# Performance work log

Hardware: AMD Instinct MI355X
Metric: run time of the kernel (lower is better)

Reference implementation:

```python
import jax, jax.numpy as jnp
import numpy as np
from jax import lax

B, T, D = 1024, 100, 12
NEG_SLOPE = 0.01  # torch.nn.LeakyReLU default


def setup_inputs() -> dict:
    key = jax.random.key(0)
    ks = jax.random.split(key, 6)
    y0 = jax.random.normal(ks[0], (B, T, D), dtype=jnp.float32)
    # shared, increasing time grid per row (forward only uses row 0, made relative)
    t = jnp.broadcast_to(jnp.linspace(0.0, 1.0, T, dtype=jnp.float32), (B, T)) + 0.0
    def lin(k, fan_in, fan_out):
        s = 1.0 / np.sqrt(fan_in)
        return jax.random.normal(k, (fan_in, fan_out), dtype=jnp.float32) * s
    W1 = lin(ks[1], D, 300); b1 = jnp.zeros((300,), jnp.float32)
    W2 = lin(ks[2], 300, 100); b2 = jnp.zeros((100,), jnp.float32)
    W3 = lin(ks[3], 100, 50); b3 = jnp.zeros((50,), jnp.float32)
    W4 = lin(ks[4], 50, D); b4 = jnp.zeros((D,), jnp.float32)
    return {"y0": y0, "t": t, "W1": W1, "b1": b1, "W2": W2, "b2": b2,
            "W3": W3, "b3": b3, "W4": W4, "b4": b4}


def _mlp(x, W1, b1, W2, b2, W3, b3, W4, b4):
    h = jax.nn.leaky_relu(x @ W1 + b1, NEG_SLOPE)
    h = jax.nn.leaky_relu(h @ W2 + b2, NEG_SLOPE)
    h = jax.nn.leaky_relu(h @ W3 + b3, NEG_SLOPE)
    return h @ W4 + b4


def reference(y0, t, W1, b1, W2, b2, W3, b3, W4, b4):
    # t_span: relative times of batch row 0 (as in the torch forward)
    t_rel = t[0] - t[0, 0]                       # [T]
    x0 = y0[:, 0, :]                             # [B, D] initial state
    f = lambda x: _mlp(x, W1, b1, W2, b2, W3, b3, W4, b4)

    def rk4_step(x, dt):
        k1 = f(x)
        k2 = f(x + 0.5 * dt * k1)
        k3 = f(x + 0.5 * dt * k2)
        k4 = f(x + dt * k3)
        x_new = x + (dt / 6.0) * (k1 + 2.0 * k2 + 2.0 * k3 + k4)
        return x_new, x_new

    dts = t_rel[1:] - t_rel[:-1]                 # [T-1]
    _, traj = lax.scan(rk4_step, x0, dts)        # [T-1, B, D]
    traj = jnp.concatenate([x0[None], traj], axis=0)  # [T, B, D]
    return jnp.swapaxes(traj, 0, 1)              # [B, T, D]
```

## Files before the change

kernel.cpp:

```cpp
#include <hip/hip_runtime.h>


typedef float v2f __attribute__((ext_vector_type(2)));
typedef float v4f __attribute__((ext_vector_type(4)));

constexpr int TT = 100;
constexpr int D  = 12;
constexpr int H1 = 300;
constexpr int H2 = 100;
constexpr int H3 = 50;
constexpr float NEG = 0.01f;

__device__ __forceinline__ float lrelu(float x) { return fmaxf(x, NEG * x); }
__device__ __forceinline__ v2f lo2(v4f v) { return __builtin_shufflevector(v, v, 0, 1); }
__device__ __forceinline__ v2f hi2(v4f v) { return __builtin_shufflevector(v, v, 2, 3); }
__device__ __forceinline__ v2f pkfma(v2f a, v2f b, v2f c) {
#if __has_builtin(__builtin_elementwise_fma)
    return __builtin_elementwise_fma(a, b, c);
#else
    return a * b + c;
#endif
}

__global__ __launch_bounds__(512)
void node_rk4_kernel(const float* __restrict__ y0, const float* __restrict__ t,
                     const float* __restrict__ W1, const float* __restrict__ b1,
                     const float* __restrict__ W2, const float* __restrict__ b2,
                     const float* __restrict__ W3, const float* __restrict__ b3,
                     const float* __restrict__ W4, const float* __restrict__ b4,
                     float* __restrict__ out)
{
    __shared__ __align__(16) float sW3c[25 * 200];
    __shared__ __align__(16) float sW4 [52 * 12];
    __shared__ __align__(16) float h1T [304 * 4];
    __shared__ __align__(16) float pL2 [32 * 104];
    __shared__ __align__(16) float h2e [4 * 104];
    __shared__ __align__(16) float h3e [4 * 52];
    __shared__ __align__(16) float sx  [48];
    __shared__ __align__(16) float sxe [48];
    __shared__ __align__(16) float sks [48];
    __shared__ float sb2[100];
    __shared__ float st [100];

    const int tid = threadIdx.x;
    const int l   = tid & 63;
    const int w   = tid >> 6;
    const bool l2act = (l < 50);

    const bool l1act = (tid < H1);
    float w1v[12];
    float rb1 = 0.0f;
#pragma unroll
    for (int k = 0; k < 12; ++k) w1v[k] = 0.0f;
    if (l1act) {
        rb1 = b1[tid];
#pragma unroll
        for (int k = 0; k < 12; ++k) w1v[k] = W1[k * H1 + tid];
    }

    float w2a[38], w2b[38];
#pragma unroll
    for (int i = 0; i < 38; ++i) {
        const int k = w * 38 + i;
        float va = 0.0f, vb = 0.0f;
        if (l2act && k < H1) { va = W2[k * H2 + l]; vb = W2[k * H2 + l + 50]; }
        w2a[i] = va; w2b[i] = vb;
    }

    const float rb3 = (w < 4 && l < 50) ? b3[l] : 0.0f;

    const int u4 = tid - 256;
    const bool l4act = (u4 >= 0 && u4 < 192);
    int e4 = 0, j4 = 0, kq4 = 0;
    float b4v = 0.0f;
    if (l4act) {
        e4 = u4 / 48; const int r = u4 - e4 * 48; j4 = r >> 2; kq4 = r & 3;
        b4v = b4[j4];
    }

    for (int i = tid; i < H2 * H3; i += 512) {
        const int k = i / H3, j = i - k * H3;
        sW3c[(k >> 2) * 200 + j * 4 + (k & 3)] = W3[i];
    }
    for (int i = tid; i < 52 * 12; i += 512) sW4[i] = (i < H3 * D) ? W4[i] : 0.0f;
    if (tid < H2) sb2[tid] = b2[tid];
    if (tid < TT) st[tid] = t[tid];
    if (tid >= 104 && tid < 120) h1T[300 * 4 + (tid - 104)] = 0.0f;
    if (tid >= 120 && tid < 128) {
        const int u = tid - 120;
        h3e[(u >> 1) * 52 + 50 + (u & 1)] = 0.0f;
    }
    if (tid < 48) {
        const int e = tid / 12, j = tid - e * 12;
        const int g = (blockIdx.x * 4 + e) * (TT * D) + j;
        const float v = y0[g];
        sx[tid] = v;
        out[g]  = v;
    }
    __syncthreads();

    for (int s = 0; s < TT - 1; ++s) {
#pragma unroll 1
        for (int ev = 0; ev < 4; ++ev) {
            const float* xin = ev ? sxe : sx;

            if (l1act) {
                v4f r;
#pragma unroll
                for (int e = 0; e < 4; ++e) {
                    const v4f x0 = *(const v4f*)(xin + e * 12);
                    const v4f x1 = *(const v4f*)(xin + e * 12 + 4);
                    const v4f x2 = *(const v4f*)(xin + e * 12 + 8);
                    float a = rb1;
                    a = fmaf(x0.x, w1v[0], a);  a = fmaf(x0.y, w1v[1], a);
                    a = fmaf(x0.z, w1v[2], a);  a = fmaf(x0.w, w1v[3], a);
                    a = fmaf(x1.x, w1v[4], a);  a = fmaf(x1.y, w1v[5], a);
                    a = fmaf(x1.z, w1v[6], a);  a = fmaf(x1.w, w1v[7], a);
                    a = fmaf(x2.x, w1v[8], a);  a = fmaf(x2.y, w1v[9], a);
                    a = fmaf(x2.z, w1v[10], a); a = fmaf(x2.w, w1v[11], a);
                    r[e] = lrelu(a);
                }
                *(v4f*)(h1T + tid * 4) = r;
            }
            __syncthreads();

            {
                v2f a01A = {0,0}, a23A = {0,0}, a01B = {0,0}, a23B = {0,0};
                const float* hb = h1T + w * (38 * 4);
#pragma unroll
                for (int i = 0; i < 38; ++i) {
                    const v4f hv = *(const v4f*)(hb + i * 4);
                    const v2f wA = {w2a[i], w2a[i]};
                    const v2f wB = {w2b[i], w2b[i]};
                    a01A = pkfma(lo2(hv), wA, a01A);
                    a23A = pkfma(hi2(hv), wA, a23A);
                    a01B = pkfma(lo2(hv), wB, a01B);
                    a23B = pkfma(hi2(hv), wB, a23B);
                }
                if (l2act) {
                    pL2[(w * 4 + 0) * 104 + l]      = a01A.x;
                    pL2[(w * 4 + 1) * 104 + l]      = a01A.y;
                    pL2[(w * 4 + 2) * 104 + l]      = a23A.x;
                    pL2[(w * 4 + 3) * 104 + l]      = a23A.y;
                    pL2[(w * 4 + 0) * 104 + l + 50] = a01B.x;
                    pL2[(w * 4 + 1) * 104 + l + 50] = a01B.y;
                    pL2[(w * 4 + 2) * 104 + l + 50] = a23B.x;
                    pL2[(w * 4 + 3) * 104 + l + 50] = a23B.y;
                }
            }
            __syncthreads();

            if (tid < 400) {
                const int e = tid / 100, j = tid - e * 100;
                float v = sb2[j];
#pragma unroll
                for (int q = 0; q < 8; ++q) v += pL2[(q * 4 + e) * 104 + j];
                h2e[e * 104 + j] = lrelu(v);
            }
            __syncthreads();

            if (w < 4 && l2act) {
                v2f acc = {0, 0};
                const float* hb2 = h2e + w * 104;
                const float* wb  = sW3c + l * 4;
#pragma unroll
                for (int c = 0; c < 25; ++c) {
                    const v4f wv = *(const v4f*)(wb + c * 200);
                    const v4f hv = *(const v4f*)(hb2 + c * 4);
                    acc = pkfma(lo2(hv), lo2(wv), acc);
                    acc = pkfma(hi2(hv), hi2(wv), acc);
                }
                h3e[w * 52 + l] = lrelu(acc.x + acc.y + rb3);
            }
            __syncthreads();

            if (l4act) {
                const int kb = kq4 * 13;
                float a = 0.0f;
                const float* hb3 = h3e + e4 * 52 + kb;
#pragma unroll
                for (int i = 0; i < 13; ++i)
                    a = fmaf(hb3[i], sW4[(kb + i) * 12 + j4], a);
                a += __shfl_xor(a, 1);
                a += __shfl_xor(a, 2);
                if (kq4 == 0) {
                    a += b4v;
                    const float dt = st[s + 1] - st[s];
                    const int bi = e4 * 12 + j4;
                    const float xc = sx[bi];
                    if (ev == 0)      { sks[bi] = a;        sxe[bi] = xc + 0.5f * dt * a; }
                    else if (ev == 1) { sks[bi] += 2.f * a; sxe[bi] = xc + 0.5f * dt * a; }
                    else if (ev == 2) { sks[bi] += 2.f * a; sxe[bi] = xc + dt * a; }
                    else {
                        const float xn = xc + dt * (1.0f / 6.0f) * (sks[bi] + a);
                        sx[bi] = xn;
                        out[(blockIdx.x * 4 + e4) * (TT * D) + (s + 1) * D + j4] = xn;
                    }
                }
            }
            __syncthreads();
        }
    }
}

extern "C" void kernel_launch(void* const* d_in, const int* in_sizes, int n_in,
                              void* d_out, int out_size, void* d_ws, size_t ws_size,
                              hipStream_t stream) {
    const float* y0 = (const float*)d_in[0];
    const float* t  = (const float*)d_in[1];
    const float* W1 = (const float*)d_in[2];
    const float* b1 = (const float*)d_in[3];
    const float* W2 = (const float*)d_in[4];
    const float* b2 = (const float*)d_in[5];
    const float* W3 = (const float*)d_in[6];
    const float* b3 = (const float*)d_in[7];
    const float* W4 = (const float*)d_in[8];
    const float* b4 = (const float*)d_in[9];
    float* out = (float*)d_out;

    node_rk4_kernel<<<256, 512, 0, stream>>>(y0, t, W1, b1, W2, b2, W3, b3, W4, b4, out);
}
```

Before: 1.308 ms.

## Double block size, split layer-2 reduction wider, fuse tail layers per wave

The block grows to 1024 threads, so each wave handles 19 rows of the layer-2 K dimension instead of 38. Partial sums are stored in an element-major layout that can be reduced with vector loads. The layer-2 reduction, layer 3, layer 4 and the RK4 update are merged into one stage run by four waves, one per batch element. This removes two block-wide barriers per function evaluation. The RK accumulator and state now live in registers instead of shared memory. The trade-off is heavier register pressure from the 1024-thread launch bound, and the tail stage relies on lockstep execution within a wave for its shared-memory handoffs.

```diff
diff --git a/kernel.cpp b/kernel.cpp
--- a/kernel.cpp
+++ b/kernel.cpp
@@ -22,7 +22,7 @@
 #endif
 }
 
-__global__ __launch_bounds__(512)
+__global__ __launch_bounds__(1024)
 void node_rk4_kernel(const float* __restrict__ y0, const float* __restrict__ t,
                      const float* __restrict__ W1, const float* __restrict__ b1,
                      const float* __restrict__ W2, const float* __restrict__ b2,
@@ -33,13 +33,11 @@
     __shared__ __align__(16) float sW3c[25 * 200];
     __shared__ __align__(16) float sW4 [52 * 12];
     __shared__ __align__(16) float h1T [304 * 4];
-    __shared__ __align__(16) float pL2 [32 * 104];
+    __shared__ __align__(16) float pL2v[4 * 100 * 20];
     __shared__ __align__(16) float h2e [4 * 104];
     __shared__ __align__(16) float h3e [4 * 52];
     __shared__ __align__(16) float sx  [48];
     __shared__ __align__(16) float sxe [48];
-    __shared__ __align__(16) float sks [48];
-    __shared__ float sb2[100];
     __shared__ float st [100];
 
     const int tid = threadIdx.x;
@@ -47,6 +45,15 @@
     const int w   = tid >> 6;
     const bool l2act = (l < 50);
 
+    float w2a[19], w2b[19];
+#pragma unroll
+    for (int i = 0; i < 19; ++i) {
+        const int k = w * 19 + i;
+        float va = 0.0f, vb = 0.0f;
+        if (l2act && k < H1) { va = W2[k * H2 + l]; vb = W2[k * H2 + l + 50]; }
+        w2a[i] = va; w2b[i] = vb;
+    }
+
     const bool l1act = (tid < H1);
     float w1v[12];
     float rb1 = 0.0f;
@@ -58,32 +65,18 @@
         for (int k = 0; k < 12; ++k) w1v[k] = W1[k * H1 + tid];
     }
 
-    float w2a[38], w2b[38];
-#pragma unroll
-    for (int i = 0; i < 38; ++i) {
-        const int k = w * 38 + i;
-        float va = 0.0f, vb = 0.0f;
-        if (l2act && k < H1) { va = W2[k * H2 + l]; vb = W2[k * H2 + l + 50]; }
-        w2a[i] = va; w2b[i] = vb;
-    }
-
-    const float rb3 = (w < 4 && l < 50) ? b3[l] : 0.0f;
-
-    const int u4 = tid - 256;
-    const bool l4act = (u4 >= 0 && u4 < 192);
-    int e4 = 0, j4 = 0, kq4 = 0;
-    float b4v = 0.0f;
-    if (l4act) {
-        e4 = u4 / 48; const int r = u4 - e4 * 48; j4 = r >> 2; kq4 = r & 3;
-        b4v = b4[j4];
-    }
-
-    for (int i = tid; i < H2 * H3; i += 512) {
+    const bool tact = (w >= 12);
+    const int  e_t  = w - 12;
+    float rb2a = 0.f, rb2b = 0.f, rb3 = 0.f;
+    if (tact && l2act) { rb2a = b2[l]; rb2b = b2[l + 50]; rb3 = b3[l]; }
+    const int j4 = l >> 2, kq4 = l & 3;
+    const float b4v = (tact && l < 48) ? b4[j4] : 0.0f;
+
+    for (int i = tid; i < H2 * H3; i += 1024) {
         const int k = i / H3, j = i - k * H3;
         sW3c[(k >> 2) * 200 + j * 4 + (k & 3)] = W3[i];
     }
-    for (int i = tid; i < 52 * 12; i += 512) sW4[i] = (i < H3 * D) ? W4[i] : 0.0f;
-    if (tid < H2) sb2[tid] = b2[tid];
+    for (int i = tid; i < 52 * 12; i += 1024) sW4[i] = (i < H3 * D) ? W4[i] : 0.0f;
     if (tid < TT) st[tid] = t[tid];
     if (tid >= 104 && tid < 120) h1T[300 * 4 + (tid - 104)] = 0.0f;
     if (tid >= 120 && tid < 128) {
@@ -99,7 +92,11 @@
     }
     __syncthreads();
 
+    float xreg = 0.0f, ks = 0.0f;
+    if (tact && l < 48 && kq4 == 0) xreg = sx[e_t * 12 + j4];
+
     for (int s = 0; s < TT - 1; ++s) {
+        const float dt = st[s + 1] - st[s];
 #pragma unroll 1
         for (int ev = 0; ev < 4; ++ev) {
             const float* xin = ev ? sxe : sx;
@@ -126,9 +123,9 @@
 
             {
                 v2f a01A = {0,0}, a23A = {0,0}, a01B = {0,0}, a23B = {0,0};
-                const float* hb = h1T + w * (38 * 4);
-#pragma unroll
-                for (int i = 0; i < 38; ++i) {
+                const float* hb = h1T + w * (19 * 4);
+#pragma unroll
+                for (int i = 0; i < 19; ++i) {
                     const v4f hv = *(const v4f*)(hb + i * 4);
                     const v2f wA = {w2a[i], w2a[i]};
                     const v2f wB = {w2b[i], w2b[i]};
@@ -138,63 +135,65 @@
                     a23B = pkfma(hi2(hv), wB, a23B);
                 }
                 if (l2act) {
-                    pL2[(w * 4 + 0) * 104 + l]      = a01A.x;
-                    pL2[(w * 4 + 1) * 104 + l]      = a01A.y;
-                    pL2[(w * 4 + 2) * 104 + l]      = a23A.x;
-                    pL2[(w * 4 + 3) * 104 + l]      = a23A.y;
-                    pL2[(w * 4 + 0) * 104 + l + 50] = a01B.x;
-                    pL2[(w * 4 + 1) * 104 + l + 50] = a01B.y;
-                    pL2[(w * 4 + 2) * 104 + l + 50] = a23B.x;
-                    pL2[(w * 4 + 3) * 104 + l + 50] = a23B.y;
+                    pL2v[(0 * 100 + l) * 20 + w]      = a01A.x;
+                    pL2v[(1 * 100 + l) * 20 + w]      = a01A.y;
+                    pL2v[(2 * 100 + l) * 20 + w]      = a23A.x;
+                    pL2v[(3 * 100 + l) * 20 + w]      = a23A.y;
+                    pL2v[(0 * 100 + l + 50) * 20 + w] = a01B.x;
+                    pL2v[(1 * 100 + l + 50) * 20 + w] = a01B.y;
+                    pL2v[(2 * 100 + l + 50) * 20 + w] = a23B.x;
+                    pL2v[(3 * 100 + l + 50) * 20 + w] = a23B.y;
                 }
             }
             __syncthreads();
 
-            if (tid < 400) {
-                const int e = tid / 100, j = tid - e * 100;
-                float v = sb2[j];
-#pragma unroll
-                for (int q = 0; q < 8; ++q) v += pL2[(q * 4 + e) * 104 + j];
-                h2e[e * 104 + j] = lrelu(v);
-            }
-            __syncthreads();
-
-            if (w < 4 && l2act) {
-                v2f acc = {0, 0};
-                const float* hb2 = h2e + w * 104;
-                const float* wb  = sW3c + l * 4;
-#pragma unroll
-                for (int c = 0; c < 25; ++c) {
-                    const v4f wv = *(const v4f*)(wb + c * 200);
-                    const v4f hv = *(const v4f*)(hb2 + c * 4);
-                    acc = pkfma(lo2(hv), lo2(wv), acc);
-                    acc = pkfma(hi2(hv), hi2(wv), acc);
-                }
-                h3e[w * 52 + l] = lrelu(acc.x + acc.y + rb3);
-            }
-            __syncthreads();
-
-            if (l4act) {
-                const int kb = kq4 * 13;
-                float a = 0.0f;
-                const float* hb3 = h3e + e4 * 52 + kb;
-#pragma unroll
-                for (int i = 0; i < 13; ++i)
-                    a = fmaf(hb3[i], sW4[(kb + i) * 12 + j4], a);
-                a += __shfl_xor(a, 1);
-                a += __shfl_xor(a, 2);
-                if (kq4 == 0) {
-                    a += b4v;
-                    const float dt = st[s + 1] - st[s];
-                    const int bi = e4 * 12 + j4;
-                    const float xc = sx[bi];
-                    if (ev == 0)      { sks[bi] = a;        sxe[bi] = xc + 0.5f * dt * a; }
-                    else if (ev == 1) { sks[bi] += 2.f * a; sxe[bi] = xc + 0.5f * dt * a; }
-                    else if (ev == 2) { sks[bi] += 2.f * a; sxe[bi] = xc + dt * a; }
-                    else {
-                        const float xn = xc + dt * (1.0f / 6.0f) * (sks[bi] + a);
-                        sx[bi] = xn;
-                        out[(blockIdx.x * 4 + e4) * (TT * D) + (s + 1) * D + j4] = xn;
+            if (tact) {
+                const int e = e_t;
+                if (l2act) {
+                    const float* pa = pL2v + (e * 100 + l) * 20;
+                    const float* pb = pL2v + (e * 100 + l + 50) * 20;
+                    const v4f A0 = *(const v4f*)(pa + 0),  A1 = *(const v4f*)(pa + 4);
+                    const v4f A2 = *(const v4f*)(pa + 8),  A3 = *(const v4f*)(pa + 12);
+                    const v4f B0 = *(const v4f*)(pb + 0),  B1 = *(const v4f*)(pb + 4);
+                    const v4f B2 = *(const v4f*)(pb + 8),  B3 = *(const v4f*)(pb + 12);
+                    const v4f SA = (A0 + A1) + (A2 + A3);
+                    const v4f SB = (B0 + B1) + (B2 + B3);
+                    const float h2a = lrelu(SA.x + SA.y + SA.z + SA.w + rb2a);
+                    const float h2b = lrelu(SB.x + SB.y + SB.z + SB.w + rb2b);
+                    h2e[e * 104 + l]      = h2a;
+                    h2e[e * 104 + l + 50] = h2b;
+                    v2f acc = {0, 0};
+                    const float* hb2 = h2e + e * 104;
+                    const float* wb  = sW3c + l * 4;
+#pragma unroll
+                    for (int c = 0; c < 25; ++c) {
+                        const v4f wv = *(const v4f*)(wb + c * 200);
+                        const v4f hv = *(const v4f*)(hb2 + c * 4);
+                        acc = pkfma(lo2(hv), lo2(wv), acc);
+                        acc = pkfma(hi2(hv), hi2(wv), acc);
+                    }
+                    h3e[e * 52 + l] = lrelu(acc.x + acc.y + rb3);
+                }
+                if (l < 48) {
+                    const int kb = kq4 * 13;
+                    float a = 0.0f;
+#pragma unroll
+                    for (int i = 0; i < 13; ++i)
+                        a = fmaf(h3e[e * 52 + kb + i], sW4[(kb + i) * 12 + j4], a);
+                    a += __shfl_xor(a, 1);
+                    a += __shfl_xor(a, 2);
+                    if (kq4 == 0) {
+                        a += b4v;
+                        const int bi = e * 12 + j4;
+                        if (ev == 0)      { ks = a;          sxe[bi] = xreg + 0.5f * dt * a; }
+                        else if (ev == 1) { ks += 2.f * a;   sxe[bi] = xreg + 0.5f * dt * a; }
+                        else if (ev == 2) { ks += 2.f * a;   sxe[bi] = xreg + dt * a; }
+                        else {
+                            const float xn = xreg + dt * (1.0f / 6.0f) * (ks + a);
+                            xreg = xn;
+                            sx[bi] = xn;
+                            out[(blockIdx.x * 4 + e) * (TT * D) + (s + 1) * D + j4] = xn;
+                        }
                     }
                 }
             }
@@ -218,5 +217,5 @@
     const float* b4 = (const float*)d_in[9];
     float* out = (float*)d_out;
 
-    node_rk4_kernel<<<256, 512, 0, stream>>>(y0, t, W1, b1, W2, b2, W3, b3, W4, b4, out);
+    node_rk4_kernel<<<256, 1024, 0, stream>>>(y0, t, W1, b1, W2, b2, W3, b3, W4, b4, out);
 }
```

New measurement: 1.757 ms. 34.3% more time.
